# Optimization experiments

Hardware: AMD Instinct MI355X
Metric: run time of the kernel (lower is better)

## Reference

```python
import jax, jax.numpy as jnp
import numpy as np

def setup_inputs() -> dict:
    key = jax.random.key(0)
    k1, k2, k3, k4 = jax.random.split(key, 4)
    B, T, C, H = 4, 4096, 1024, 64
    x = jax.random.normal(k1, (B, T, C), dtype=jnp.float32)
    Wk = jax.random.normal(k2, (C, H), dtype=jnp.float32) * (C ** -0.5)
    Wq = jax.random.normal(k3, (C, H), dtype=jnp.float32) * (C ** -0.5)
    Wv = jax.random.normal(k4, (C, H), dtype=jnp.float32) * (C ** -0.5)
    return {"x": x, "Wk": Wk, "Wq": Wq, "Wv": Wv}

def reference(x, Wk, Wq, Wv):
    B, T, C = x.shape
    k = x @ Wk          # [B,T,H]
    q = x @ Wq          # [B,T,H]
    v = x @ Wv          # [B,T,H]
    # NOTE: original scales by C**-0.5 (full embed dim), not head_size**-0.5
    scale = C ** -0.5
    wei = jnp.einsum('bqh,bkh->bqk', q, k) * scale          # [B,T,T]
    causal = jnp.tril(jnp.ones((T, T), dtype=bool))
    wei = jnp.where(causal, wei, -jnp.inf)
    wei = jax.nn.softmax(wei, axis=-1)
    # dropout is identity in eval mode
    out = jnp.einsum('bqk,bkh->bqh', wei, v)                # [B,T,H]
    return out
```

## Files before the change

### kernel.cpp

```cpp
#include <hip/hip_runtime.h>
#include <hip/hip_bf16.h>
#include <stdint.h>

#define T_SEQ 4096
#define CDIM 1024
#define HDIM 64
#define M0 4.0f

typedef __attribute__((ext_vector_type(8))) short short8;
typedef __attribute__((ext_vector_type(4))) short short4v;
typedef __attribute__((ext_vector_type(8))) __bf16 bf16x8;
typedef __attribute__((ext_vector_type(4))) float f32x4;

static __device__ __forceinline__ short f2bf(float f) {
    uint32_t u = __builtin_bit_cast(uint32_t, f);
    u += 0x7FFFu + ((u >> 16) & 1u);
    return (short)(u >> 16);
}

static __device__ __forceinline__ f32x4 mfma16(short8 a, short8 b, f32x4 c) {
    return __builtin_amdgcn_mfma_f32_16x16x32_bf16(
        __builtin_bit_cast(bf16x8, a), __builtin_bit_cast(bf16x8, b), c, 0, 0, 0);
}

__global__ void prep_w2(const float* __restrict__ Wk, const float* __restrict__ Wq,
                        const float* __restrict__ Wv, short* __restrict__ W2) {
    const int d = blockIdx.x * 256 + threadIdx.x;
    const int j = d & 7, l = (d >> 3) & 63;
    const int f = d >> 9;
    const int nt2 = f % 12, rest = f / 12;
    const int i = rest & 15, s = rest >> 4;
    const int n = s * 96 + (nt2 >> 1) * 16 + (l & 15);
    const int k = i * 64 + (nt2 & 1) * 32 + ((l >> 4) << 3) + j;
    float v;
    if (n < 64)       v = Wq[k * 64 + n] * (0.03125f * 1.44269504088896340736f);
    else if (n < 128) v = Wk[k * 64 + (n - 64)];
    else              v = Wv[k * 64 + (n - 128)];
    W2[d] = f2bf(v);
}

__global__ __launch_bounds__(256) void proj(const float* __restrict__ x,
                                            const short* __restrict__ W2,
                                            short* __restrict__ Qo,
                                            short* __restrict__ Ko,
                                            short* __restrict__ VT) {
    __shared__ __align__(16) short tX[2][2048];
    const int tid = threadIdx.x;
    const int lane = tid & 63, wave = tid >> 6;
    const int r = lane & 15, g = lane >> 4;
    const int msub = wave >> 1, nsplit = wave & 1;
    const int m0 = blockIdx.x * 32;

    const int srow = tid >> 3, sc = tid & 7;
    const float* xgp = x + (size_t)(m0 + srow) * CDIM + sc * 8;
    short* xd = &tX[0][srow * 64 + ((sc ^ (srow & 7)) << 3)];
    const int bufstride = 2048;

    const int arow = msub * 16 + r;
    const int aoff0 = arow * 64 + (((0 + g) ^ (arow & 7)) << 3);
    const int aoff1 = arow * 64 + (((4 + g) ^ (arow & 7)) << 3);

    const short* w2base = W2 + (size_t)nsplit * 16 * 6144 + lane * 8;

    f32x4 acc[6];
    #pragma unroll
    for (int i = 0; i < 6; ++i) acc[i] = (f32x4){0.f, 0.f, 0.f, 0.f};

    short8 wA[12], wB[12];
    {
        const short* wp = w2base;
        #pragma unroll
        for (int f = 0; f < 12; ++f) wA[f] = *(const short8*)(wp + f * 512);
    }

    f32x4 a0 = *(const f32x4*)(xgp);
    f32x4 a1 = *(const f32x4*)(xgp + 4);
    {
        short8 v;
        #pragma unroll
        for (int q = 0; q < 4; ++q) { v[q] = f2bf(a0[q]); v[4 + q] = f2bf(a1[q]); }
        *(short8*)xd = v;
    }
    a0 = *(const f32x4*)(xgp + 64);
    a1 = *(const f32x4*)(xgp + 64 + 4);
    __syncthreads();

    auto step = [&](int i, short8 (&WC)[12], short8 (&WN)[12]) {
        if (i + 1 < 16) {
            const short* wp = w2base + (size_t)(i + 1) * 6144;
            #pragma unroll
            for (int f = 0; f < 12; ++f) WN[f] = *(const short8*)(wp + f * 512);
        }
        if (i + 1 < 16) {
            short8 v;
            #pragma unroll
            for (int q = 0; q < 4; ++q) { v[q] = f2bf(a0[q]); v[4 + q] = f2bf(a1[q]); }
            *(short8*)(xd + ((i & 1) ? 0 : bufstride)) = v;
        }
        if (i + 2 < 16) {
            a0 = *(const f32x4*)(xgp + (i + 2) * 64);
            a1 = *(const f32x4*)(xgp + (i + 2) * 64 + 4);
        }
        const short* Xt = &tX[i & 1][0];
        short8 xf0 = *(const short8*)(Xt + aoff0);
        short8 xf1 = *(const short8*)(Xt + aoff1);
        #pragma unroll
        for (int nt = 0; nt < 6; ++nt) {
            if (nsplit == 1 && nt >= 2) {
                acc[nt] = mfma16(WC[2 * nt], xf0, acc[nt]);
                acc[nt] = mfma16(WC[2 * nt + 1], xf1, acc[nt]);
            } else {
                acc[nt] = mfma16(xf0, WC[2 * nt], acc[nt]);
                acc[nt] = mfma16(xf1, WC[2 * nt + 1], acc[nt]);
            }
        }
        __syncthreads();
    };

    for (int ii = 0; ii < 16; ii += 2) {
        step(ii, wA, wB);
        step(ii + 1, wB, wA);
    }

    const int b = m0 >> 12;
    const int tb = m0 & (T_SEQ - 1);
    if (nsplit == 0) {
        #pragma unroll
        for (int nt = 0; nt < 4; ++nt)
            #pragma unroll
            for (int rr = 0; rr < 4; ++rr)
                Qo[(size_t)(m0 + msub * 16 + g * 4 + rr) * HDIM + nt * 16 + r] = f2bf(acc[nt][rr]);
        #pragma unroll
        for (int nt = 4; nt < 6; ++nt)
            #pragma unroll
            for (int rr = 0; rr < 4; ++rr)
                Ko[(size_t)(m0 + msub * 16 + g * 4 + rr) * HDIM + (nt - 4) * 16 + r] = f2bf(acc[nt][rr]);
    } else {
        #pragma unroll
        for (int nt = 0; nt < 2; ++nt)
            #pragma unroll
            for (int rr = 0; rr < 4; ++rr)
                Ko[(size_t)(m0 + msub * 16 + g * 4 + rr) * HDIM + 32 + nt * 16 + r] = f2bf(acc[nt][rr]);
        const int kpanel = tb >> 6;
        const int kk0 = (tb & 63) + msub * 16;
        #pragma unroll
        for (int nt = 2; nt < 6; ++nt)
            #pragma unroll
            for (int rr = 0; rr < 4; ++rr) {
                const int h = (nt - 2) * 16 + g * 4 + rr;
                VT[(((size_t)b * 64 + kpanel) * 64 + h) * 64 + kk0 + r] = f2bf(acc[nt][rr]);
            }
    }
}

__global__ __launch_bounds__(256) void attn(const short* __restrict__ Q,
                                            const short* __restrict__ K,
                                            const short* __restrict__ VT,
                                            float* __restrict__ out,
                                            float* __restrict__ opart,
                                            float* __restrict__ lpart) {
    __shared__ __align__(16) short tK[2][4096];
    __shared__ __align__(16) short tV[2][2][2304];

    const int tid = threadIdx.x;
    const int lane = tid & 63, wave = tid >> 6;
    const int r = lane & 15, g = lane >> 4;
    const int b = blockIdx.x & 3;
    const int s = (int)(blockIdx.x >> 2) & 3;
    const int u = (int)(blockIdx.x >> 4);
    const int quad = u >> 4, v5 = u & 15;
    int qt;
    if (quad == 0)      qt = 63 - v5;
    else if (quad == 1) qt = v5;
    else if (quad == 2) qt = 47 - v5;
    else                qt = 16 + v5;
    const int qs = qt * 64 + wave * 16;
    const int n64 = qt + 1;
    const int niters = (n64 > s) ? ((n64 - s + 3) >> 2) : 0;

    const short* Qb = Q + (size_t)b * T_SEQ * HDIM;
    const short* Kb = K + (size_t)b * T_SEQ * HDIM;
    const short* Vb = VT + (size_t)b * 64 * 64 * 64;

    short8 qf0 = *(const short8*)(Qb + (qs + r) * HDIM + g * 8);
    short8 qf1 = *(const short8*)(Qb + (qs + r) * HDIM + 32 + g * 8);

    const int srow = tid >> 2, sc = tid & 3;
    const short* kgp = Kb + (s * 64 + srow) * HDIM + sc * 8;
    const short* vgp = Vb + s * 4096 + srow * 64 + sc * 8;
    short* kda = &tK[0][srow * 64 + ((sc ^ (srow & 7)) << 3)];
    short* kdb = &tK[0][srow * 64 + (((sc + 4) ^ (srow & 7)) << 3)];
    short* vda = &tV[0][0][srow * 36 + sc * 8];
    short* vdb = &tV[0][1][srow * 36 + sc * 8];
    const int KBUF = 4096;
    const int VBUF = 2 * 2304;

    const short* K0 = &tK[0][0]; const short* K1 = &tK[1][0];
    const short* V0 = &tV[0][0][0]; const short* V1 = &tV[1][0][0];
    int kfo0[4], kfo1[4];
    #pragma unroll
    for (int kk = 0; kk < 4; ++kk) {
        kfo0[kk] = (kk * 16 + r) * 64 + (((0 + g) ^ (r & 7)) << 3);
        kfo1[kk] = (kk * 16 + r) * 64 + (((4 + g) ^ (r & 7)) << 3);
    }
    int voA[4];
    #pragma unroll
    for (int ht = 0; ht < 4; ++ht) voA[ht] = (ht * 16 + r) * 36 + g * 4;

    float lrun = 0.f;
    f32x4 o[4];
    #pragma unroll
    for (int i = 0; i < 4; ++i) o[i] = (f32x4){0.f, 0.f, 0.f, 0.f};
    const int tq = qs + r;

    if (niters > 0) {
        short8 krega = *(const short8*)kgp;
        short8 kregb = *(const short8*)(kgp + 32);
        short8 vrega = *(const short8*)vgp;
        short8 vregb = *(const short8*)(vgp + 32);
        *(short8*)kda = krega;  *(short8*)kdb = kregb;
        *(short8*)vda = vrega;  *(short8*)vdb = vregb;
        if (niters > 1) {
            krega = *(const short8*)(kgp + 16384);
            kregb = *(const short8*)(kgp + 16384 + 32);
            vrega = *(const short8*)(vgp + 16384);
            vregb = *(const short8*)(vgp + 16384 + 32);
        }
        __syncthreads();

        for (int i = 0; i < niters; ++i) {
            if (i + 1 < niters) {
                const int offK = (i & 1) ? 0 : KBUF;
                const int offV = (i & 1) ? 0 : VBUF;
                *(short8*)(kda + offK) = krega;  *(short8*)(kdb + offK) = kregb;
                *(short8*)(vda + offV) = vrega;  *(short8*)(vdb + offV) = vregb;
            }
            if (i + 2 < niters) {
                krega = *(const short8*)(kgp + (size_t)(i + 2) * 16384);
                kregb = *(const short8*)(kgp + (size_t)(i + 2) * 16384 + 32);
                vrega = *(const short8*)(vgp + (size_t)(i + 2) * 16384);
                vregb = *(const short8*)(vgp + (size_t)(i + 2) * 16384 + 32);
            }
            const int ktm = (4 * i + s) * 64;
            const short* Kt  = (i & 1) ? K1 : K0;
            const short* Vt0 = (i & 1) ? V1 : V0;
            const short* Vt1 = Vt0 + 2304;

            short8 pf[2];
            __builtin_amdgcn_s_setprio(1);
            #pragma unroll
            for (int kk = 0; kk < 4; ++kk) {
                short8 kf0 = *(const short8*)(Kt + kfo0[kk]);
                short8 kf1 = *(const short8*)(Kt + kfo1[kk]);
                f32x4 sv4 = mfma16(kf0, qf0, (f32x4){0.f, 0.f, 0.f, 0.f});
                sv4 = mfma16(kf1, qf1, sv4);
                #pragma unroll
                for (int rr = 0; rr < 4; ++rr) {
                    const int kg = ktm + kk * 16 + g * 4 + rr;
                    float sv = sv4[rr];
                    sv = (kg <= tq) ? sv : -1e30f;
                    const float pv = __builtin_amdgcn_exp2f(sv - M0);
                    lrun += pv;
                    pf[kk >> 1][(kk & 1) * 4 + rr] = f2bf(pv);
                }
            }
            #pragma unroll
            for (int ht = 0; ht < 4; ++ht) {
                #pragma unroll
                for (int w2 = 0; w2 < 2; ++w2) {
                    const short* Vt = w2 ? Vt1 : Vt0;
                    short4v lo = *(const short4v*)(Vt + voA[ht]);
                    short4v hi = *(const short4v*)(Vt + voA[ht] + 16);
                    short8 vf;
                    #pragma unroll
                    for (int q4 = 0; q4 < 4; ++q4) { vf[q4] = lo[q4]; vf[4 + q4] = hi[q4]; }
                    o[ht] = mfma16(vf, pf[w2], o[ht]);
                }
            }
            __builtin_amdgcn_s_setprio(0);
            __syncthreads();
        }
    }

    lrun += __shfl_xor(lrun, 16);
    lrun += __shfl_xor(lrun, 32);
    const int row = (b << 12) + qs + r;
    if (g == 0) lpart[s * 16384 + row] = lrun;
    float* ob = (s == 0 ? out : opart + (size_t)(s - 1) * 16384 * HDIM) + (size_t)row * HDIM;
    #pragma unroll
    for (int ht = 0; ht < 4; ++ht)
        *(f32x4*)(ob + ht * 16 + g * 4) = o[ht];
}

__global__ __launch_bounds__(256) void norm4(float* __restrict__ out,
                                             const float* __restrict__ opart,
                                             const float* __restrict__ lpart) {
    const int i4 = blockIdx.x * 256 + threadIdx.x;
    const int row = i4 >> 4;
    f32x4 v = *(const f32x4*)(out + (size_t)i4 * 4);
    #pragma unroll
    for (int s = 0; s < 3; ++s)
        v += *(const f32x4*)(opart + (size_t)s * 16384 * HDIM + (size_t)i4 * 4);
    const float inv = 1.0f / (lpart[row] + lpart[16384 + row] +
                              lpart[2 * 16384 + row] + lpart[3 * 16384 + row]);
    v *= inv;
    *(f32x4*)(out + (size_t)i4 * 4) = v;
}

extern "C" void kernel_launch(void* const* d_in, const int* in_sizes, int n_in,
                              void* d_out, int out_size, void* d_ws, size_t ws_size,
                              hipStream_t stream) {
    const float* x  = (const float*)d_in[0];
    const float* Wk = (const float*)d_in[1];
    const float* Wq = (const float*)d_in[2];
    const float* Wv = (const float*)d_in[3];
    float* out = (float*)d_out;

    char* ws = (char*)d_ws;
    short* W2 = (short*)ws;
    short* Qb = (short*)(ws + 393216);
    short* Kb = (short*)(ws + 393216 + 2097152);
    short* VT = (short*)(ws + 393216 + 2 * 2097152);
    float* opart = (float*)(ws + 393216 + 3 * 2097152);
    float* lpart = (float*)(ws + 393216 + 3 * 2097152 + 3 * 4194304);

    prep_w2<<<768, 256, 0, stream>>>(Wk, Wq, Wv, W2);
    proj<<<512, 256, 0, stream>>>(x, W2, Qb, Kb, VT);
    attn<<<1024, 256, 0, stream>>>(Qb, Kb, VT, out, opart, lpart);
    norm4<<<1024, 256, 0, stream>>>(out, opart, lpart);
}
```

Before: 58.58 us.

## Stream K/V tiles directly into LDS with global_load_lds and swizzled V layout

Replaces the register-staged global→LDS copy of K and V tiles with direct global_load_lds 16-byte transfers, removing the two-iteration register prefetch and the explicit LDS stores. The V tile layout changes from padded rows (stride 36) to an XOR-swizzled 64-wide layout so the direct-to-LDS writes and the MFMA fragment reads stay conflict-light. This cuts VGPR pressure and VALU/LDS store instructions, but prefetch depth drops to one tile ahead, so load latency may be less hidden.

```diff
diff --git a/kernel.cpp b/kernel.cpp
--- a/kernel.cpp
+++ b/kernel.cpp
@@ -21,6 +21,12 @@
 static __device__ __forceinline__ f32x4 mfma16(short8 a, short8 b, f32x4 c) {
     return __builtin_amdgcn_mfma_f32_16x16x32_bf16(
         __builtin_bit_cast(bf16x8, a), __builtin_bit_cast(bf16x8, b), c, 0, 0, 0);
+}
+
+static __device__ __forceinline__ void gload_lds16(const void* g, void* l) {
+    __builtin_amdgcn_global_load_lds(
+        (const __attribute__((address_space(1))) void*)g,
+        (__attribute__((address_space(3))) void*)l, 16, 0, 0);
 }
 
 __global__ void prep_w2(const float* __restrict__ Wk, const float* __restrict__ Wq,
@@ -160,7 +166,7 @@
                                             float* __restrict__ opart,
                                             float* __restrict__ lpart) {
     __shared__ __align__(16) short tK[2][4096];
-    __shared__ __align__(16) short tV[2][2][2304];
+    __shared__ __align__(16) short tV[2][4096];
 
     const int tid = threadIdx.x;
     const int lane = tid & 63, wave = tid >> 6;
@@ -185,27 +191,29 @@
     short8 qf0 = *(const short8*)(Qb + (qs + r) * HDIM + g * 8);
     short8 qf1 = *(const short8*)(Qb + (qs + r) * HDIM + 32 + g * 8);
 
-    const int srow = tid >> 2, sc = tid & 3;
-    const short* kgp = Kb + (s * 64 + srow) * HDIM + sc * 8;
-    const short* vgp = Vb + s * 4096 + srow * 64 + sc * 8;
-    short* kda = &tK[0][srow * 64 + ((sc ^ (srow & 7)) << 3)];
-    short* kdb = &tK[0][srow * 64 + (((sc + 4) ^ (srow & 7)) << 3)];
-    short* vda = &tV[0][0][srow * 36 + sc * 8];
-    short* vdb = &tV[0][1][srow * 36 + sc * 8];
-    const int KBUF = 4096;
-    const int VBUF = 2 * 2304;
-
-    const short* K0 = &tK[0][0]; const short* K1 = &tK[1][0];
-    const short* V0 = &tV[0][0][0]; const short* V1 = &tV[1][0][0];
+    const int lrow = lane >> 3;
+    const int lchk = (lane & 7) ^ lrow;
+    const short* kgp0 = Kb + (size_t)(s * 64 + wave * 16 + lrow) * 64 + lchk * 8;
+    const short* kgp1 = Kb + (size_t)(s * 64 + wave * 16 + 8 + lrow) * 64 + lchk * 8;
+    const short* vgp0 = Vb + (size_t)s * 4096 + (wave * 16 + lrow) * 64 + lchk * 8;
+    const short* vgp1 = Vb + (size_t)s * 4096 + (wave * 16 + 8 + lrow) * 64 + lchk * 8;
+    const int ldso0 = (wave * 2) * 512, ldso1 = (wave * 2 + 1) * 512;
+
     int kfo0[4], kfo1[4];
     #pragma unroll
     for (int kk = 0; kk < 4; ++kk) {
         kfo0[kk] = (kk * 16 + r) * 64 + (((0 + g) ^ (r & 7)) << 3);
         kfo1[kk] = (kk * 16 + r) * 64 + (((4 + g) ^ (r & 7)) << 3);
     }
-    int voA[4];
-    #pragma unroll
-    for (int ht = 0; ht < 4; ++ht) voA[ht] = (ht * 16 + r) * 36 + g * 4;
+    int voL[2][4], voH[2][4];
+    #pragma unroll
+    for (int w2 = 0; w2 < 2; ++w2)
+        #pragma unroll
+        for (int ht = 0; ht < 4; ++ht) {
+            const int h = ht * 16 + r;
+            voL[w2][ht] = h * 64 + (((w2 * 4 + (g >> 1)) ^ (r & 7)) << 3) + (g & 1) * 4;
+            voH[w2][ht] = h * 64 + (((w2 * 4 + 2 + (g >> 1)) ^ (r & 7)) << 3) + (g & 1) * 4;
+        }
 
     float lrun = 0.f;
     f32x4 o[4];
@@ -214,37 +222,24 @@
     const int tq = qs + r;
 
     if (niters > 0) {
-        short8 krega = *(const short8*)kgp;
-        short8 kregb = *(const short8*)(kgp + 32);
-        short8 vrega = *(const short8*)vgp;
-        short8 vregb = *(const short8*)(vgp + 32);
-        *(short8*)kda = krega;  *(short8*)kdb = kregb;
-        *(short8*)vda = vrega;  *(short8*)vdb = vregb;
-        if (niters > 1) {
-            krega = *(const short8*)(kgp + 16384);
-            kregb = *(const short8*)(kgp + 16384 + 32);
-            vrega = *(const short8*)(vgp + 16384);
-            vregb = *(const short8*)(vgp + 16384 + 32);
-        }
+        gload_lds16(kgp0, &tK[0][ldso0]);
+        gload_lds16(kgp1, &tK[0][ldso1]);
+        gload_lds16(vgp0, &tV[0][ldso0]);
+        gload_lds16(vgp1, &tV[0][ldso1]);
         __syncthreads();
 
         for (int i = 0; i < niters; ++i) {
             if (i + 1 < niters) {
-                const int offK = (i & 1) ? 0 : KBUF;
-                const int offV = (i & 1) ? 0 : VBUF;
-                *(short8*)(kda + offK) = krega;  *(short8*)(kdb + offK) = kregb;
-                *(short8*)(vda + offV) = vrega;  *(short8*)(vdb + offV) = vregb;
-            }
-            if (i + 2 < niters) {
-                krega = *(const short8*)(kgp + (size_t)(i + 2) * 16384);
-                kregb = *(const short8*)(kgp + (size_t)(i + 2) * 16384 + 32);
-                vrega = *(const short8*)(vgp + (size_t)(i + 2) * 16384);
-                vregb = *(const short8*)(vgp + (size_t)(i + 2) * 16384 + 32);
+                const int bn = (i + 1) & 1;
+                const size_t adv = (size_t)(i + 1) * 16384;
+                gload_lds16(kgp0 + adv, &tK[bn][ldso0]);
+                gload_lds16(kgp1 + adv, &tK[bn][ldso1]);
+                gload_lds16(vgp0 + adv, &tV[bn][ldso0]);
+                gload_lds16(vgp1 + adv, &tV[bn][ldso1]);
             }
             const int ktm = (4 * i + s) * 64;
-            const short* Kt  = (i & 1) ? K1 : K0;
-            const short* Vt0 = (i & 1) ? V1 : V0;
-            const short* Vt1 = Vt0 + 2304;
+            const short* Kt = &tK[i & 1][0];
+            const short* Vt = &tV[i & 1][0];
 
             short8 pf[2];
             __builtin_amdgcn_s_setprio(1);
@@ -268,9 +263,8 @@
             for (int ht = 0; ht < 4; ++ht) {
                 #pragma unroll
                 for (int w2 = 0; w2 < 2; ++w2) {
-                    const short* Vt = w2 ? Vt1 : Vt0;
-                    short4v lo = *(const short4v*)(Vt + voA[ht]);
-                    short4v hi = *(const short4v*)(Vt + voA[ht] + 16);
+                    short4v lo = *(const short4v*)(Vt + voL[w2][ht]);
+                    short4v hi = *(const short4v*)(Vt + voH[w2][ht]);
                     short8 vf;
                     #pragma unroll
                     for (int q4 = 0; q4 < 4; ++q4) { vf[q4] = lo[q4]; vf[4 + q4] = hi[q4]; }
```

Result: faster. 56.58 us (-3.4%).
